# Performance work log

Measured on AMD Instinct MI355X. Metric: run time of the kernel, lower is better.

## Reference

```python
import jax, jax.numpy as jnp
import numpy as np

N_NODES = 50000
IN_DIM = 256
OUT_DIM = 128
NNZ_FEAT = 800000
NNZ_ADJ = 800000


def setup_inputs() -> dict:
    key = jax.random.key(0)
    ks = jax.random.split(key, 10)
    inp = {
        "feat_row": jax.random.randint(ks[0], (NNZ_FEAT,), 0, N_NODES, dtype=jnp.int32),
        "feat_col": jax.random.randint(ks[1], (NNZ_FEAT,), 0, IN_DIM, dtype=jnp.int32),
        "feat_vals": jnp.ones((NNZ_FEAT,), dtype=jnp.float32),  # binary features (int-cast in original)
        "adj1_row": jax.random.randint(ks[2], (NNZ_ADJ,), 0, N_NODES, dtype=jnp.int32),
        "adj1_col": jax.random.randint(ks[3], (NNZ_ADJ,), 0, N_NODES, dtype=jnp.int32),
        "adj1_vals": jax.random.uniform(ks[4], (NNZ_ADJ,), dtype=jnp.float32),
        "adj2_row": jax.random.randint(ks[5], (NNZ_ADJ,), 0, N_NODES, dtype=jnp.int32),
        "adj2_col": jax.random.randint(ks[6], (NNZ_ADJ,), 0, N_NODES, dtype=jnp.int32),
        "adj2_vals": jax.random.uniform(ks[7], (NNZ_ADJ,), dtype=jnp.float32),
    }
    # Glorot-uniform weights as in weight_variable_glorot
    lim = np.sqrt(6.0 / (IN_DIM + OUT_DIM))
    inp["W1"] = jax.random.uniform(ks[8], (IN_DIM, OUT_DIM), minval=-lim, maxval=lim, dtype=jnp.float32)
    inp["W2"] = jax.random.uniform(ks[9], (IN_DIM, OUT_DIM), minval=-lim, maxval=lim, dtype=jnp.float32)
    inp["n_nodes"] = N_NODES
    return inp


def _spmm_feat(row, col, vals, W, n_nodes):
    # X (sparse [N, F]) @ W ([F, D]) -> [N, D]
    msg = vals[:, None] * W[col]  # [nnz, D]
    return jax.ops.segment_sum(msg, row, num_segments=n_nodes)


def _spmm_adj(row, col, vals, H, n_nodes):
    # A (sparse [N, N]) @ H ([N, D]) -> [N, D]
    msg = vals[:, None] * H[col]  # [E, D]
    return jax.ops.segment_sum(msg, row, num_segments=n_nodes)


def reference(feat_row, feat_col, feat_vals, adj1_row, adj1_col, adj1_vals,
              adj2_row, adj2_col, adj2_vals, W1, W2, n_nodes):
    # dropout=0.0 -> keep_prob=1 -> sparse dropout is identity with scale 1.0
    xw1 = _spmm_feat(feat_row, feat_col, feat_vals, W1, n_nodes)   # [N, D]
    x1 = _spmm_adj(adj1_row, adj1_col, adj1_vals, xw1, n_nodes)    # [N, D]
    xw2 = _spmm_feat(feat_row, feat_col, feat_vals, W2, n_nodes)
    x2 = _spmm_adj(adj2_row, adj2_col, adj2_vals, xw2, n_nodes)
    return jax.nn.relu(x1 + x2)
```

## Files before the change

### kernel.cpp

```cpp
#include <hip/hip_runtime.h>
#include <hip/hip_fp16.h>

#define N_NODES 50000
#define IN_DIM 256
#define OUT_DIM 128
#define NNZ 800000
#define SCAN_N (3 * N_NODES)
#define TOTAL_NNZ (3 * NNZ)
#define SCAN_BLOCKS ((SCAN_N + 255) / 256)
#define NPART 8
#define PART_W (N_NODES / NPART)

#define BCAP 310016

#define NSUB 64
#define SUBW 98
#define SUBCAP 6144
#define ENT_B 4096
#define BBLK_B ((BCAP + ENT_B - 1) / ENT_B)

#define ADJ_SL 4
#define ADJ_RC ((N_NODES + 63) / 64)

typedef float vf4 __attribute__((ext_vector_type(4)));

static __device__ __forceinline__ unsigned pack_cv(int c, float v) {
    return ((unsigned)c << 16) | (unsigned)__half_as_ushort(__float2half(v));
}
static __device__ __forceinline__ int   upk_c(unsigned pk) { return (int)(pk >> 16); }
static __device__ __forceinline__ float upk_v(unsigned pk) {
    return __half2float(__ushort_as_half((unsigned short)(pk & 0xffffu)));
}
static __device__ __forceinline__ float h2f(unsigned short h) {
    return __half2float(__ushort_as_half(h));
}

__global__ void bucket_kernel(const int* __restrict__ fr, const int* __restrict__ fc,
                              const float* __restrict__ fv,
                              const int* __restrict__ a1r, const int* __restrict__ a1c,
                              const float* __restrict__ a1v,
                              const int* __restrict__ a2r, const int* __restrict__ a2c,
                              const float* __restrict__ a2v,
                              int* __restrict__ bcur,
                              unsigned* __restrict__ gpack,
                              unsigned short* __restrict__ gmeta) {
    __shared__ int cnt8[8];
    __shared__ int offc[8];
    __shared__ int gbase[8];
    __shared__ unsigned spk[768];
    __shared__ unsigned short smeta[768];
    int t = threadIdx.x;
    if (t < 8) cnt8[t] = 0;
    __syncthreads();

    int e = blockIdx.x * 256 + t;
    int r[3]; unsigned pk[3]; int loc[3]; int pb[3];
    r[0] = __builtin_nontemporal_load(&fr[e]);
    pk[0] = pack_cv(__builtin_nontemporal_load(&fc[e]),
                    __builtin_nontemporal_load(&fv[e]));
    r[1] = __builtin_nontemporal_load(&a1r[e]);
    pk[1] = pack_cv(__builtin_nontemporal_load(&a1c[e]),
                    __builtin_nontemporal_load(&a1v[e]));
    r[2] = __builtin_nontemporal_load(&a2r[e]);
    pk[2] = pack_cv(__builtin_nontemporal_load(&a2c[e]),
                    __builtin_nontemporal_load(&a2v[e]));
#pragma unroll
    for (int s = 0; s < 3; ++s) {
        pb[s] = r[s] / PART_W;
        loc[s] = atomicAdd(&cnt8[pb[s]], 1);
    }
    __syncthreads();
    if (t < 8) gbase[t] = atomicAdd(&bcur[t], cnt8[t]);
    if (t == 0) {
        int acc = 0;
#pragma unroll
        for (int q = 0; q < 8; ++q) { offc[q] = acc; acc += cnt8[q]; }
    }
    __syncthreads();
#pragma unroll
    for (int s = 0; s < 3; ++s) {
        int pos = offc[pb[s]] + loc[s];
        spk[pos] = pk[s];
        smeta[pos] = (unsigned short)((s << 13) | (r[s] - pb[s] * PART_W));
    }
    __syncthreads();
#pragma unroll
    for (int k = 0; k < 3; ++k) {
        int i = t + k * 256;
        int q = 0;
#pragma unroll
        for (int b = 1; b < 8; ++b) q += (i >= offc[b]);
        int g = q * BCAP + gbase[q] + (i - offc[q]);
        gpack[g] = spk[i];
        gmeta[g] = smeta[i];
    }
}

__global__ void subbucket_kernel(const unsigned* __restrict__ gpack1,
                                 const unsigned short* __restrict__ gmeta1,
                                 const int* __restrict__ bcur,
                                 int* __restrict__ subcur,
                                 unsigned* __restrict__ gpack2,
                                 unsigned short* __restrict__ gmeta2) {
    int p = blockIdx.x & (NPART - 1);
    int chunk = blockIdx.x >> 3;
    int base = chunk * ENT_B;
    int n = bcur[p];
    int cnt = n - base;
    if (cnt <= 0) return;
    if (cnt > ENT_B) cnt = ENT_B;
    __shared__ int c64[NSUB], off[NSUB], gb[NSUB];
    __shared__ unsigned spk[ENT_B];
    __shared__ unsigned short smt[ENT_B];
    int t = threadIdx.x;
    if (t < NSUB) c64[t] = 0;
    __syncthreads();
    unsigned pk[16]; unsigned short mt[16]; int loc[16]; int sb[16];
#pragma unroll
    for (int k = 0; k < 16; ++k) {
        int i = t + k * 256;
        if (i < cnt) {
            pk[k] = gpack1[p * BCAP + base + i];
            mt[k] = gmeta1[p * BCAP + base + i];
            sb[k] = (int)(mt[k] & 8191u) / SUBW;
            loc[k] = atomicAdd(&c64[sb[k]], 1);
        } else sb[k] = -1;
    }
    __syncthreads();
    if (t == 0) {
        int a = 0;
#pragma unroll
        for (int q = 0; q < NSUB; ++q) { off[q] = a; a += c64[q]; }
    }
    __syncthreads();
    if (t < NSUB && c64[t] > 0) gb[t] = atomicAdd(&subcur[p * NSUB + t], c64[t]);
    __syncthreads();
#pragma unroll
    for (int k = 0; k < 16; ++k) {
        if (sb[k] >= 0) {
            int pos = off[sb[k]] + loc[k];
            spk[pos] = pk[k];
            smt[pos] = mt[k];
        }
    }
    __syncthreads();
    for (int i = t; i < cnt; i += 256) {
        unsigned short m = smt[i];
        int s2 = (int)(m & 8191u) / SUBW;
        int g = (p * NSUB + s2) * SUBCAP + gb[s2] + (i - off[s2]);
        gpack2[g] = spk[i];
        gmeta2[g] = m;
    }
}

__global__ __launch_bounds__(512) void subhist_kernel(
        const unsigned short* __restrict__ gmeta2,
        const int* __restrict__ subcur,
        int* __restrict__ cnt) {
    int p = blockIdx.x & (NPART - 1);
    int sub = blockIdx.x >> 3;
    int n = subcur[p * NSUB + sub];
    __shared__ int h[512];
    int t = threadIdx.x;
    h[t] = 0;
    __syncthreads();
    long base = (long)(p * NSUB + sub) * SUBCAP;
    for (int i = t; i < n; i += 512) {
        unsigned short m = gmeta2[base + i];
        int key = (int)(m >> 13) * SUBW + ((int)(m & 8191u) - sub * SUBW);
        atomicAdd(&h[key], 1);
    }
    __syncthreads();
    if (t < 3 * SUBW) {
        int s = t / SUBW, d = t - s * SUBW;
        int rl = sub * SUBW + d;
        if (rl < PART_W) cnt[s * N_NODES + p * PART_W + rl] = h[t];
    }
}

__global__ void scan_block_kernel(const int* __restrict__ cnt,
                                  int* __restrict__ starts,
                                  int* __restrict__ bsum) {
    __shared__ int tmp[256];
    int g = blockIdx.x * 256 + threadIdx.x;
    int v = (g < SCAN_N) ? cnt[g] : 0;
    tmp[threadIdx.x] = v;
    __syncthreads();
    for (int off = 1; off < 256; off <<= 1) {
        int t = (threadIdx.x >= off) ? tmp[threadIdx.x - off] : 0;
        __syncthreads();
        tmp[threadIdx.x] += t;
        __syncthreads();
    }
    int incl = tmp[threadIdx.x];
    if (g < SCAN_N) starts[g] = incl - v;
    if (threadIdx.x == 255) bsum[blockIdx.x] = incl;
}

__global__ void scan_bsum_kernel(int* __restrict__ bsum, int nb) {
    __shared__ int tmp[1024];
    int t = threadIdx.x;
    int v = (t < nb) ? bsum[t] : 0;
    tmp[t] = v;
    __syncthreads();
    for (int off = 1; off < 1024; off <<= 1) {
        int x = (t >= off) ? tmp[t - off] : 0;
        __syncthreads();
        tmp[t] += x;
        __syncthreads();
    }
    if (t < nb) bsum[t] = tmp[t] - v;
}

__global__ void scan_add_kernel(int* __restrict__ starts,
                                const int* __restrict__ bsum) {
    int g = blockIdx.x * 256 + threadIdx.x;
    if (g < SCAN_N) starts[g] += bsum[blockIdx.x];
}

__global__ __launch_bounds__(512) void sort_write_kernel(
        const unsigned* __restrict__ gpack2,
        const unsigned short* __restrict__ gmeta2,
        const int* __restrict__ subcur,
        const int* __restrict__ starts,
        unsigned* __restrict__ spack) {
    int p = blockIdx.x & (NPART - 1);
    int sub = blockIdx.x >> 3;
    int n = subcur[p * NSUB + sub];
    __shared__ int h[512];
    __shared__ int e[512];
    __shared__ int cur[512];
    __shared__ unsigned sorted[SUBCAP];
    int t = threadIdx.x;
    h[t] = 0;
    __syncthreads();
    long base = (long)(p * NSUB + sub) * SUBCAP;
    unsigned pk[12]; short ky[12];
#pragma unroll
    for (int k = 0; k < 12; ++k) {
        int i = t + k * 512;
        if (i < n) {
            pk[k] = gpack2[base + i];
            unsigned short m = gmeta2[base + i];
            int key = (int)(m >> 13) * SUBW + ((int)(m & 8191u) - sub * SUBW);
            ky[k] = (short)key;
            atomicAdd(&h[key], 1);
        } else ky[k] = -1;
    }
    __syncthreads();
    e[t] = h[t];
    __syncthreads();
    for (int off = 1; off < 512; off <<= 1) {
        int v = (t >= off) ? e[t - off] : 0;
        __syncthreads();
        e[t] += v;
        __syncthreads();
    }
    int excl = e[t] - h[t];
    __syncthreads();
    e[t] = excl;
    cur[t] = excl;
    __syncthreads();
#pragma unroll
    for (int k = 0; k < 12; ++k) {
        if (ky[k] >= 0) {
            int pos = atomicAdd(&cur[ky[k]], 1);
            sorted[pos] = pk[k];
        }
    }
    __syncthreads();
    int s1 = e[SUBW];
    int s2 = e[2 * SUBW];
    int rb = p * PART_W + sub * SUBW;
    int gb0 = starts[rb];
    int gb1 = starts[N_NODES + rb];
    int gb2 = starts[2 * N_NODES + rb];
#pragma unroll
    for (int k = 0; k < 12; ++k) {
        int i = t + k * 512;
        if (i < n) {
            unsigned v = sorted[i];
            int dst;
            if (i < s1)      dst = gb0 + i;
            else if (i < s2) dst = gb1 + (i - s1);
            else             dst = gb2 + (i - s2);
            spack[dst] = v;
        }
    }
}

__global__ void feat_gather_kernel(const int* __restrict__ starts,
                                   const unsigned* __restrict__ spack,
                                   const float4* __restrict__ W1,
                                   const float4* __restrict__ W2,
                                   ushort4* __restrict__ xw1s,
                                   ushort4* __restrict__ xw2s) {
    int lane = threadIdx.x & 31;
    int sub  = threadIdx.x >> 5;
    int r = blockIdx.x * 8 + sub;
    if (r >= N_NODES) return;
    int s = starts[r];
    int e = starts[r + 1];
    float4 a1 = make_float4(0.f, 0.f, 0.f, 0.f);
    float4 a2 = make_float4(0.f, 0.f, 0.f, 0.f);
    for (int base = s; base < e; base += 32) {
        int n = e - base;
        int m = (n < 32) ? n : 32;
        unsigned pk = (lane < m) ? spack[base + lane] : 0u;
        int j = 0;
        for (; j + 7 < m; j += 8) {
            unsigned pp[8]; float4 w1v[8]; float4 w2v[8];
#pragma unroll
            for (int k = 0; k < 8; ++k) pp[k] = __shfl(pk, j + k, 32);
#pragma unroll
            for (int k = 0; k < 8; ++k) {
                int c = upk_c(pp[k]);
                w1v[k] = W1[c * 32 + lane];
                w2v[k] = W2[c * 32 + lane];
            }
#pragma unroll
            for (int k = 0; k < 8; ++k) {
                float v = upk_v(pp[k]);
                a1.x += v * w1v[k].x; a1.y += v * w1v[k].y;
                a1.z += v * w1v[k].z; a1.w += v * w1v[k].w;
                a2.x += v * w2v[k].x; a2.y += v * w2v[k].y;
                a2.z += v * w2v[k].z; a2.w += v * w2v[k].w;
            }
        }
        for (; j + 3 < m; j += 4) {
            unsigned pp[4]; float4 w1v[4]; float4 w2v[4];
#pragma unroll
            for (int k = 0; k < 4; ++k) pp[k] = __shfl(pk, j + k, 32);
#pragma unroll
            for (int k = 0; k < 4; ++k) {
                int c = upk_c(pp[k]);
                w1v[k] = W1[c * 32 + lane];
                w2v[k] = W2[c * 32 + lane];
            }
#pragma unroll
            for (int k = 0; k < 4; ++k) {
                float v = upk_v(pp[k]);
                a1.x += v * w1v[k].x; a1.y += v * w1v[k].y;
                a1.z += v * w1v[k].z; a1.w += v * w1v[k].w;
                a2.x += v * w2v[k].x; a2.y += v * w2v[k].y;
                a2.z += v * w2v[k].z; a2.w += v * w2v[k].w;
            }
        }
        for (; j < m; ++j) {
            unsigned pj = __shfl(pk, j, 32);
            int c = upk_c(pj);
            float v = upk_v(pj);
            float4 w1 = W1[c * 32 + lane];
            float4 w2 = W2[c * 32 + lane];
            a1.x += v * w1.x; a1.y += v * w1.y; a1.z += v * w1.z; a1.w += v * w1.w;
            a2.x += v * w2.x; a2.y += v * w2.y; a2.z += v * w2.z; a2.w += v * w2.w;
        }
    }
    ushort4 q1, q2;
    q1.x = __half_as_ushort(__float2half(a1.x)); q1.y = __half_as_ushort(__float2half(a1.y));
    q1.z = __half_as_ushort(__float2half(a1.z)); q1.w = __half_as_ushort(__float2half(a1.w));
    q2.x = __half_as_ushort(__float2half(a2.x)); q2.y = __half_as_ushort(__float2half(a2.y));
    q2.z = __half_as_ushort(__float2half(a2.z)); q2.w = __half_as_ushort(__float2half(a2.w));
    size_t idx = (size_t)(lane >> 3) * (N_NODES * 8) + (size_t)r * 8 + (lane & 7);
    xw1s[idx] = q1;
    xw2s[idx] = q2;
}

__global__ __launch_bounds__(512) void adj_pass_rel0(
        const int* __restrict__ starts,
        const unsigned* __restrict__ spack,
        const ushort4* __restrict__ xws,
        vf4* __restrict__ out) {
    int s  = blockIdx.x & (ADJ_SL - 1);
    int rc = blockIdx.x >> 2;
    int g  = threadIdx.x >> 3;
    int q  = threadIdx.x & 7;
    int r  = rc * 64 + g;
    bool valid = (r < N_NODES);
    vf4 acc = {0.f, 0.f, 0.f, 0.f};
    const ushort4* __restrict__ sl = xws + (size_t)s * (N_NODES * 8);
    size_t oidx = (size_t)r * 32 + s * 8 + q;

    int st = 0, en = 0;
    if (valid) {
        st = starts[N_NODES + r];
        en = starts[N_NODES + r + 1];
    }
    for (int base = st; base < en; base += 16) {
        int m = en - base;
        unsigned pk0 = (q < m)     ? spack[base + q]     : 0u;
        unsigned pk1 = (8 + q < m) ? spack[base + 8 + q] : 0u;
        {
            unsigned pp[8]; ushort4 xx[8];
#pragma unroll
            for (int k = 0; k < 8; ++k) pp[k] = __shfl(pk0, k, 8);
#pragma unroll
            for (int k = 0; k < 8; ++k) xx[k] = sl[upk_c(pp[k]) * 8 + q];
#pragma unroll
            for (int k = 0; k < 8; ++k) {
                float v = upk_v(pp[k]);
                acc.x += v * h2f(xx[k].x); acc.y += v * h2f(xx[k].y);
                acc.z += v * h2f(xx[k].z); acc.w += v * h2f(xx[k].w);
            }
        }
        if (m <= 8) continue;
        {
            unsigned pp[8]; ushort4 xx[8];
#pragma unroll
            for (int k = 0; k < 8; ++k) pp[k] = __shfl(pk1, k, 8);
#pragma unroll
            for (int k = 0; k < 8; ++k) xx[k] = sl[upk_c(pp[k]) * 8 + q];
#pragma unroll
            for (int k = 0; k < 8; ++k) {
                float v = upk_v(pp[k]);
                acc.x += v * h2f(xx[k].x); acc.y += v * h2f(xx[k].y);
                acc.z += v * h2f(xx[k].z); acc.w += v * h2f(xx[k].w);
            }
        }
    }
    if (valid) __builtin_nontemporal_store(acc, &out[oidx]);
}

__global__ __launch_bounds__(512) void adj_pass_rel1(
        const int* __restrict__ starts,
        const unsigned* __restrict__ spack,
        const ushort4* __restrict__ xws,
        vf4* __restrict__ out) {
    int s  = blockIdx.x & (ADJ_SL - 1);
    int rc = blockIdx.x >> 2;
    int g  = threadIdx.x >> 3;
    int q  = threadIdx.x & 7;
    int r  = rc * 64 + g;
    bool valid = (r < N_NODES);
    vf4 acc = {0.f, 0.f, 0.f, 0.f};
    const ushort4* __restrict__ sl = xws + (size_t)s * (N_NODES * 8);
    size_t oidx = (size_t)r * 32 + s * 8 + q;

    int st = 0, en = 0;
    if (valid) {
        st = starts[2 * N_NODES + r];
        en = (r == N_NODES - 1) ? TOTAL_NNZ : starts[2 * N_NODES + r + 1];
    }
    vf4 prev = {0.f, 0.f, 0.f, 0.f};
    if (valid) prev = __builtin_nontemporal_load(&out[oidx]);

    for (int base = st; base < en; base += 16) {
        int m = en - base;
        unsigned pk0 = (q < m)     ? spack[base + q]     : 0u;
        unsigned pk1 = (8 + q < m) ? spack[base + 8 + q] : 0u;
        {
            unsigned pp[8]; ushort4 xx[8];
#pragma unroll
            for (int k = 0; k < 8; ++k) pp[k] = __shfl(pk0, k, 8);
#pragma unroll
            for (int k = 0; k < 8; ++k) xx[k] = sl[upk_c(pp[k]) * 8 + q];
#pragma unroll
            for (int k = 0; k < 8; ++k) {
                float v = upk_v(pp[k]);
                acc.x += v * h2f(xx[k].x); acc.y += v * h2f(xx[k].y);
                acc.z += v * h2f(xx[k].z); acc.w += v * h2f(xx[k].w);
            }
        }
        if (m <= 8) continue;
        {
            unsigned pp[8]; ushort4 xx[8];
#pragma unroll
            for (int k = 0; k < 8; ++k) pp[k] = __shfl(pk1, k, 8);
#pragma unroll
            for (int k = 0; k < 8; ++k) xx[k] = sl[upk_c(pp[k]) * 8 + q];
#pragma unroll
            for (int k = 0; k < 8; ++k) {
                float v = upk_v(pp[k]);
                acc.x += v * h2f(xx[k].x); acc.y += v * h2f(xx[k].y);
                acc.z += v * h2f(xx[k].z); acc.w += v * h2f(xx[k].w);
            }
        }
    }
    if (valid) {
        vf4 res;
        res.x = fmaxf(acc.x + prev.x, 0.f);
        res.y = fmaxf(acc.y + prev.y, 0.f);
        res.z = fmaxf(acc.z + prev.z, 0.f);
        res.w = fmaxf(acc.w + prev.w, 0.f);
        __builtin_nontemporal_store(res, &out[oidx]);
    }
}

extern "C" void kernel_launch(void* const* d_in, const int* in_sizes, int n_in,
                              void* d_out, int out_size, void* d_ws, size_t ws_size,
                              hipStream_t stream) {
    const int*   feat_row  = (const int*)  d_in[0];
    const int*   feat_col  = (const int*)  d_in[1];
    const float* feat_vals = (const float*)d_in[2];
    const int*   adj1_row  = (const int*)  d_in[3];
    const int*   adj1_col  = (const int*)  d_in[4];
    const float* adj1_vals = (const float*)d_in[5];
    const int*   adj2_row  = (const int*)  d_in[6];
    const int*   adj2_col  = (const int*)  d_in[7];
    const float* adj2_vals = (const float*)d_in[8];
    const float* W1        = (const float*)d_in[9];
    const float* W2        = (const float*)d_in[10];

    char* ws = (char*)d_ws;
    unsigned* spack = (unsigned*)ws;            ws += (size_t)TOTAL_NNZ * 4;
    int*      cnt   = (int*)ws;                 ws += (size_t)SCAN_N * 4;
    int*      starts= (int*)ws;                 ws += (size_t)SCAN_N * 4;
    int*      bsum  = (int*)ws;                 ws += 1024 * 4;
    int*      bcur  = (int*)ws;                 ws += 16 * 4;
    int*      subcur= (int*)ws;                 ws += (size_t)NPART * NSUB * 4;
    char*     bkt   = ws;
    unsigned* gpack1 = (unsigned*)bkt;
    unsigned short* gmeta1 = (unsigned short*)(bkt + (size_t)NPART * BCAP * 4);
    unsigned* gpack2 = (unsigned*)(bkt + (size_t)NPART * BCAP * 6);
    unsigned short* gmeta2 = (unsigned short*)(bkt + (size_t)NPART * BCAP * 6
                                                  + (size_t)NPART * NSUB * SUBCAP * 4);
    ushort4*  xw1s  = (ushort4*)bkt;
    ushort4*  xw2s  = (ushort4*)(bkt + (size_t)N_NODES * OUT_DIM * 2);

    (void)hipMemsetAsync(bcur, 0, (16 + NPART * NSUB) * sizeof(int), stream);

    const int block = 256;

    bucket_kernel<<<NNZ / block, block, 0, stream>>>(
        feat_row, feat_col, feat_vals,
        adj1_row, adj1_col, adj1_vals,
        adj2_row, adj2_col, adj2_vals,
        bcur, gpack1, gmeta1);

    subbucket_kernel<<<NPART * BBLK_B, block, 0, stream>>>(
        gpack1, gmeta1, bcur, subcur, gpack2, gmeta2);

    subhist_kernel<<<NPART * NSUB, 512, 0, stream>>>(gmeta2, subcur, cnt);

    scan_block_kernel<<<SCAN_BLOCKS, 256, 0, stream>>>(cnt, starts, bsum);
    scan_bsum_kernel<<<1, 1024, 0, stream>>>(bsum, SCAN_BLOCKS);
    scan_add_kernel<<<SCAN_BLOCKS, 256, 0, stream>>>(starts, bsum);

    sort_write_kernel<<<NPART * NSUB, 512, 0, stream>>>(
        gpack2, gmeta2, subcur, starts, spack);

    const int grid_rows = N_NODES / 8;
    feat_gather_kernel<<<grid_rows, 256, 0, stream>>>(
        starts, spack, (const float4*)W1, (const float4*)W2, xw1s, xw2s);

    adj_pass_rel0<<<ADJ_SL * ADJ_RC, 512, 0, stream>>>(
        starts, spack, xw1s, (vf4*)d_out);
    adj_pass_rel1<<<ADJ_SL * ADJ_RC, 512, 0, stream>>>(
        starts, spack, xw2s, (vf4*)d_out);
}
```

Measured before the change: 264.9 us.

## Densify feature matrix and compute X@W with MFMA instead of sparse gather

The sparse feature matrix is scattered with atomics into a dense fp32 N×256 buffer, and X@[W1|W2] is computed with fp16 MFMA 16x16x32 instructions. Feature nonzeros no longer go through the bucket/sort pipeline, which now handles only the two adjacency relations, so the buckets and scan are smaller. In exchange it adds a 51 MB memset, an atomic scatter and a dense GEMM read of that buffer. It also rounds X to fp16, which is exact for the binary test features but lossy for general values.

```diff
diff --git a/kernel.cpp b/kernel.cpp
--- a/kernel.cpp
+++ b/kernel.cpp
@@ -5,17 +5,17 @@
 #define IN_DIM 256
 #define OUT_DIM 128
 #define NNZ 800000
-#define SCAN_N (3 * N_NODES)
-#define TOTAL_NNZ (3 * NNZ)
+#define N_ADJ_TOT (2 * NNZ)
+#define SCAN_N (2 * N_NODES)
 #define SCAN_BLOCKS ((SCAN_N + 255) / 256)
 #define NPART 8
 #define PART_W (N_NODES / NPART)
 
-#define BCAP 310016
+#define BCAP 208128
 
 #define NSUB 64
 #define SUBW 98
-#define SUBCAP 6144
+#define SUBCAP 4096
 #define ENT_B 4096
 #define BBLK_B ((BCAP + ENT_B - 1) / ENT_B)
 
@@ -23,6 +23,8 @@
 #define ADJ_RC ((N_NODES + 63) / 64)
 
 typedef float vf4 __attribute__((ext_vector_type(4)));
+typedef float f32x4a __attribute__((ext_vector_type(4)));
+typedef _Float16 f16x8 __attribute__((ext_vector_type(8)));
 
 static __device__ __forceinline__ unsigned pack_cv(int c, float v) {
     return ((unsigned)c << 16) | (unsigned)__half_as_ushort(__float2half(v));
@@ -35,9 +37,83 @@
     return __half2float(__ushort_as_half(h));
 }
 
-__global__ void bucket_kernel(const int* __restrict__ fr, const int* __restrict__ fc,
-                              const float* __restrict__ fv,
-                              const int* __restrict__ a1r, const int* __restrict__ a1c,
+__global__ void densify_kernel(const int* __restrict__ fr,
+                               const int* __restrict__ fc,
+                               const float* __restrict__ fv,
+                               float* __restrict__ X) {
+    int e = blockIdx.x * 256 + threadIdx.x;
+    int r = __builtin_nontemporal_load(&fr[e]);
+    int c = __builtin_nontemporal_load(&fc[e]);
+    float v = __builtin_nontemporal_load(&fv[e]);
+    atomicAdd(&X[(size_t)r * IN_DIM + c], v);
+}
+
+__global__ void bprep_kernel(const float* __restrict__ W1,
+                             const float* __restrict__ W2,
+                             f16x8* __restrict__ Bfrag) {
+    int idx = blockIdx.x * 256 + threadIdx.x;
+    int tk = idx >> 6, l = idx & 63;
+    int ct = tk >> 3, kk = tk & 7;
+    int col = ct * 16 + (l & 15);
+    int kb = kk * 32 + ((l >> 4) << 3);
+    f16x8 b;
+#pragma unroll
+    for (int i = 0; i < 8; ++i) {
+        int k = kb + i;
+        float w = (col < OUT_DIM) ? W1[k * OUT_DIM + col]
+                                  : W2[k * OUT_DIM + (col - OUT_DIM)];
+        b[i] = (_Float16)w;
+    }
+    Bfrag[tk * 64 + l] = b;
+}
+
+__global__ __launch_bounds__(256) void feat_mfma_kernel(
+        const float* __restrict__ X,
+        const f16x8* __restrict__ Bfrag,
+        __half* __restrict__ xw1h,
+        __half* __restrict__ xw2h) {
+    int r0 = blockIdx.x * 16;
+    int w = threadIdx.x >> 6, l = threadIdx.x & 63;
+    f32x4a acc0 = {0.f,0.f,0.f,0.f}, acc1 = {0.f,0.f,0.f,0.f};
+    f32x4a acc2 = {0.f,0.f,0.f,0.f}, acc3 = {0.f,0.f,0.f,0.f};
+    int row = r0 + (l & 15);
+    const float* ap = X + (size_t)row * IN_DIM + ((l >> 4) << 3);
+#pragma unroll
+    for (int kk = 0; kk < 8; ++kk) {
+        const float4* a4 = (const float4*)(ap + kk * 32);
+        float4 x0 = a4[0];
+        float4 x1 = a4[1];
+        f16x8 a;
+        a[0] = (_Float16)x0.x; a[1] = (_Float16)x0.y;
+        a[2] = (_Float16)x0.z; a[3] = (_Float16)x0.w;
+        a[4] = (_Float16)x1.x; a[5] = (_Float16)x1.y;
+        a[6] = (_Float16)x1.z; a[7] = (_Float16)x1.w;
+        f16x8 b0 = Bfrag[((4 * w + 0) * 8 + kk) * 64 + l];
+        f16x8 b1 = Bfrag[((4 * w + 1) * 8 + kk) * 64 + l];
+        f16x8 b2 = Bfrag[((4 * w + 2) * 8 + kk) * 64 + l];
+        f16x8 b3 = Bfrag[((4 * w + 3) * 8 + kk) * 64 + l];
+        acc0 = __builtin_amdgcn_mfma_f32_16x16x32_f16(a, b0, acc0, 0, 0, 0);
+        acc1 = __builtin_amdgcn_mfma_f32_16x16x32_f16(a, b1, acc1, 0, 0, 0);
+        acc2 = __builtin_amdgcn_mfma_f32_16x16x32_f16(a, b2, acc2, 0, 0, 0);
+        acc3 = __builtin_amdgcn_mfma_f32_16x16x32_f16(a, b3, acc3, 0, 0, 0);
+    }
+#pragma unroll
+    for (int ct = 0; ct < 4; ++ct) {
+        f32x4a acc = (ct == 0) ? acc0 : (ct == 1) ? acc1 : (ct == 2) ? acc2 : acc3;
+        int col = (4 * w + ct) * 16 + (l & 15);
+        int dim = col & (OUT_DIM - 1);
+        __half* base = (col < OUT_DIM) ? xw1h : xw2h;
+        int slice = dim >> 5, within = dim & 31;
+        size_t sb = (size_t)slice * N_NODES * 32 + within;
+#pragma unroll
+        for (int j = 0; j < 4; ++j) {
+            int rr = r0 + ((l >> 4) << 2) + j;
+            base[sb + (size_t)rr * 32] = __float2half(acc[j]);
+        }
+    }
+}
+
+__global__ void bucket_kernel(const int* __restrict__ a1r, const int* __restrict__ a1c,
                               const float* __restrict__ a1v,
                               const int* __restrict__ a2r, const int* __restrict__ a2c,
                               const float* __restrict__ a2v,
@@ -47,25 +123,22 @@
     __shared__ int cnt8[8];
     __shared__ int offc[8];
     __shared__ int gbase[8];
-    __shared__ unsigned spk[768];
-    __shared__ unsigned short smeta[768];
+    __shared__ unsigned spk[512];
+    __shared__ unsigned short smeta[512];
     int t = threadIdx.x;
     if (t < 8) cnt8[t] = 0;
     __syncthreads();
 
     int e = blockIdx.x * 256 + t;
-    int r[3]; unsigned pk[3]; int loc[3]; int pb[3];
-    r[0] = __builtin_nontemporal_load(&fr[e]);
-    pk[0] = pack_cv(__builtin_nontemporal_load(&fc[e]),
-                    __builtin_nontemporal_load(&fv[e]));
-    r[1] = __builtin_nontemporal_load(&a1r[e]);
-    pk[1] = pack_cv(__builtin_nontemporal_load(&a1c[e]),
+    int r[2]; unsigned pk[2]; int loc[2]; int pb[2];
+    r[0] = __builtin_nontemporal_load(&a1r[e]);
+    pk[0] = pack_cv(__builtin_nontemporal_load(&a1c[e]),
                     __builtin_nontemporal_load(&a1v[e]));
-    r[2] = __builtin_nontemporal_load(&a2r[e]);
-    pk[2] = pack_cv(__builtin_nontemporal_load(&a2c[e]),
+    r[1] = __builtin_nontemporal_load(&a2r[e]);
+    pk[1] = pack_cv(__builtin_nontemporal_load(&a2c[e]),
                     __builtin_nontemporal_load(&a2v[e]));
 #pragma unroll
-    for (int s = 0; s < 3; ++s) {
+    for (int s = 0; s < 2; ++s) {
         pb[s] = r[s] / PART_W;
         loc[s] = atomicAdd(&cnt8[pb[s]], 1);
     }
@@ -78,14 +151,14 @@
     }
     __syncthreads();
 #pragma unroll
-    for (int s = 0; s < 3; ++s) {
+    for (int s = 0; s < 2; ++s) {
         int pos = offc[pb[s]] + loc[s];
         spk[pos] = pk[s];
         smeta[pos] = (unsigned short)((s << 13) | (r[s] - pb[s] * PART_W));
     }
     __syncthreads();
 #pragma unroll
-    for (int k = 0; k < 3; ++k) {
+    for (int k = 0; k < 2; ++k) {
         int i = t + k * 256;
         int q = 0;
 #pragma unroll
@@ -171,7 +244,7 @@
         atomicAdd(&h[key], 1);
     }
     __syncthreads();
-    if (t < 3 * SUBW) {
+    if (t < 2 * SUBW) {
         int s = t / SUBW, d = t - s * SUBW;
         int rl = sub * SUBW + d;
         if (rl < PART_W) cnt[s * N_NODES + p * PART_W + rl] = h[t];
@@ -235,9 +308,9 @@
     h[t] = 0;
     __syncthreads();
     long base = (long)(p * NSUB + sub) * SUBCAP;
-    unsigned pk[12]; short ky[12];
-#pragma unroll
-    for (int k = 0; k < 12; ++k) {
+    unsigned pk[8]; short ky[8];
+#pragma unroll
+    for (int k = 0; k < 8; ++k) {
         int i = t + k * 512;
         if (i < n) {
             pk[k] = gpack2[base + i];
@@ -262,7 +335,7 @@
     cur[t] = excl;
     __syncthreads();
 #pragma unroll
-    for (int k = 0; k < 12; ++k) {
+    for (int k = 0; k < 8; ++k) {
         if (ky[k] >= 0) {
             int pos = atomicAdd(&cur[ky[k]], 1);
             sorted[pos] = pk[k];
@@ -270,100 +343,18 @@
     }
     __syncthreads();
     int s1 = e[SUBW];
-    int s2 = e[2 * SUBW];
     int rb = p * PART_W + sub * SUBW;
     int gb0 = starts[rb];
     int gb1 = starts[N_NODES + rb];
-    int gb2 = starts[2 * N_NODES + rb];
-#pragma unroll
-    for (int k = 0; k < 12; ++k) {
+#pragma unroll
+    for (int k = 0; k < 8; ++k) {
         int i = t + k * 512;
         if (i < n) {
             unsigned v = sorted[i];
-            int dst;
-            if (i < s1)      dst = gb0 + i;
-            else if (i < s2) dst = gb1 + (i - s1);
-            else             dst = gb2 + (i - s2);
+            int dst = (i < s1) ? (gb0 + i) : (gb1 + (i - s1));
             spack[dst] = v;
         }
     }
-}
-
-__global__ void feat_gather_kernel(const int* __restrict__ starts,
-                                   const unsigned* __restrict__ spack,
-                                   const float4* __restrict__ W1,
-                                   const float4* __restrict__ W2,
-                                   ushort4* __restrict__ xw1s,
-                                   ushort4* __restrict__ xw2s) {
-    int lane = threadIdx.x & 31;
-    int sub  = threadIdx.x >> 5;
-    int r = blockIdx.x * 8 + sub;
-    if (r >= N_NODES) return;
-    int s = starts[r];
-    int e = starts[r + 1];
-    float4 a1 = make_float4(0.f, 0.f, 0.f, 0.f);
-    float4 a2 = make_float4(0.f, 0.f, 0.f, 0.f);
-    for (int base = s; base < e; base += 32) {
-        int n = e - base;
-        int m = (n < 32) ? n : 32;
-        unsigned pk = (lane < m) ? spack[base + lane] : 0u;
-        int j = 0;
-        for (; j + 7 < m; j += 8) {
-            unsigned pp[8]; float4 w1v[8]; float4 w2v[8];
-#pragma unroll
-            for (int k = 0; k < 8; ++k) pp[k] = __shfl(pk, j + k, 32);
-#pragma unroll
-            for (int k = 0; k < 8; ++k) {
-                int c = upk_c(pp[k]);
-                w1v[k] = W1[c * 32 + lane];
-                w2v[k] = W2[c * 32 + lane];
-            }
-#pragma unroll
-            for (int k = 0; k < 8; ++k) {
-                float v = upk_v(pp[k]);
-                a1.x += v * w1v[k].x; a1.y += v * w1v[k].y;
-                a1.z += v * w1v[k].z; a1.w += v * w1v[k].w;
-                a2.x += v * w2v[k].x; a2.y += v * w2v[k].y;
-                a2.z += v * w2v[k].z; a2.w += v * w2v[k].w;
-            }
-        }
-        for (; j + 3 < m; j += 4) {
-            unsigned pp[4]; float4 w1v[4]; float4 w2v[4];
-#pragma unroll
-            for (int k = 0; k < 4; ++k) pp[k] = __shfl(pk, j + k, 32);
-#pragma unroll
-            for (int k = 0; k < 4; ++k) {
-                int c = upk_c(pp[k]);
-                w1v[k] = W1[c * 32 + lane];
-                w2v[k] = W2[c * 32 + lane];
-            }
-#pragma unroll
-            for (int k = 0; k < 4; ++k) {
-                float v = upk_v(pp[k]);
-                a1.x += v * w1v[k].x; a1.y += v * w1v[k].y;
-                a1.z += v * w1v[k].z; a1.w += v * w1v[k].w;
-                a2.x += v * w2v[k].x; a2.y += v * w2v[k].y;
-                a2.z += v * w2v[k].z; a2.w += v * w2v[k].w;
-            }
-        }
-        for (; j < m; ++j) {
-            unsigned pj = __shfl(pk, j, 32);
-            int c = upk_c(pj);
-            float v = upk_v(pj);
-            float4 w1 = W1[c * 32 + lane];
-            float4 w2 = W2[c * 32 + lane];
-            a1.x += v * w1.x; a1.y += v * w1.y; a1.z += v * w1.z; a1.w += v * w1.w;
-            a2.x += v * w2.x; a2.y += v * w2.y; a2.z += v * w2.z; a2.w += v * w2.w;
-        }
-    }
-    ushort4 q1, q2;
-    q1.x = __half_as_ushort(__float2half(a1.x)); q1.y = __half_as_ushort(__float2half(a1.y));
-    q1.z = __half_as_ushort(__float2half(a1.z)); q1.w = __half_as_ushort(__float2half(a1.w));
-    q2.x = __half_as_ushort(__float2half(a2.x)); q2.y = __half_as_ushort(__float2half(a2.y));
-    q2.z = __half_as_ushort(__float2half(a2.z)); q2.w = __half_as_ushort(__float2half(a2.w));
-    size_t idx = (size_t)(lane >> 3) * (N_NODES * 8) + (size_t)r * 8 + (lane & 7);
-    xw1s[idx] = q1;
-    xw2s[idx] = q2;
 }
 
 __global__ __launch_bounds__(512) void adj_pass_rel0(
@@ -383,8 +374,8 @@
 
     int st = 0, en = 0;
     if (valid) {
-        st = starts[N_NODES + r];
-        en = starts[N_NODES + r + 1];
+        st = starts[r];
+        en = starts[r + 1];
     }
     for (int base = st; base < en; base += 16) {
         int m = en - base;
@@ -438,8 +429,8 @@
 
     int st = 0, en = 0;
     if (valid) {
-        st = starts[2 * N_NODES + r];
-        en = (r == N_NODES - 1) ? TOTAL_NNZ : starts[2 * N_NODES + r + 1];
+        st = starts[N_NODES + r];
+        en = (r == N_NODES - 1) ? N_ADJ_TOT : starts[N_NODES + r + 1];
     }
     vf4 prev = {0.f, 0.f, 0.f, 0.f};
     if (valid) prev = __builtin_nontemporal_load(&out[oidx]);
@@ -502,49 +493,48 @@
     const float* W2        = (const float*)d_in[10];
 
     char* ws = (char*)d_ws;
-    unsigned* spack = (unsigned*)ws;            ws += (size_t)TOTAL_NNZ * 4;
+    unsigned* spack = (unsigned*)ws;            ws += (size_t)N_ADJ_TOT * 4;
     int*      cnt   = (int*)ws;                 ws += (size_t)SCAN_N * 4;
     int*      starts= (int*)ws;                 ws += (size_t)SCAN_N * 4;
     int*      bsum  = (int*)ws;                 ws += 1024 * 4;
     int*      bcur  = (int*)ws;                 ws += 16 * 4;
     int*      subcur= (int*)ws;                 ws += (size_t)NPART * NSUB * 4;
+    float*    X     = (float*)ws;               ws += (size_t)N_NODES * IN_DIM * 4;
+    f16x8*    Bfrag = (f16x8*)ws;               ws += (size_t)128 * 64 * 16;
     char*     bkt   = ws;
     unsigned* gpack1 = (unsigned*)bkt;
     unsigned short* gmeta1 = (unsigned short*)(bkt + (size_t)NPART * BCAP * 4);
     unsigned* gpack2 = (unsigned*)(bkt + (size_t)NPART * BCAP * 6);
     unsigned short* gmeta2 = (unsigned short*)(bkt + (size_t)NPART * BCAP * 6
                                                   + (size_t)NPART * NSUB * SUBCAP * 4);
-    ushort4*  xw1s  = (ushort4*)bkt;
-    ushort4*  xw2s  = (ushort4*)(bkt + (size_t)N_NODES * OUT_DIM * 2);
+    __half*   xw1h  = (__half*)bkt;
+    __half*   xw2h  = (__half*)(bkt + (size_t)N_NODES * OUT_DIM * 2);
 
     (void)hipMemsetAsync(bcur, 0, (16 + NPART * NSUB) * sizeof(int), stream);
+    (void)hipMemsetAsync(X, 0, (size_t)N_NODES * IN_DIM * sizeof(float), stream);
 
     const int block = 256;
 
+    densify_kernel<<<NNZ / block, block, 0, stream>>>(feat_row, feat_col, feat_vals, X);
+    bprep_kernel<<<32, block, 0, stream>>>(W1, W2, Bfrag);
+
     bucket_kernel<<<NNZ / block, block, 0, stream>>>(
-        feat_row, feat_col, feat_vals,
         adj1_row, adj1_col, adj1_vals,
         adj2_row, adj2_col, adj2_vals,
         bcur, gpack1, gmeta1);
-
     subbucket_kernel<<<NPART * BBLK_B, block, 0, stream>>>(
         gpack1, gmeta1, bcur, subcur, gpack2, gmeta2);
-
     subhist_kernel<<<NPART * NSUB, 512, 0, stream>>>(gmeta2, subcur, cnt);
-
     scan_block_kernel<<<SCAN_BLOCKS, 256, 0, stream>>>(cnt, starts, bsum);
     scan_bsum_kernel<<<1, 1024, 0, stream>>>(bsum, SCAN_BLOCKS);
     scan_add_kernel<<<SCAN_BLOCKS, 256, 0, stream>>>(starts, bsum);
-
     sort_write_kernel<<<NPART * NSUB, 512, 0, stream>>>(
         gpack2, gmeta2, subcur, starts, spack);
 
-    const int grid_rows = N_NODES / 8;
-    feat_gather_kernel<<<grid_rows, 256, 0, stream>>>(
-        starts, spack, (const float4*)W1, (const float4*)W2, xw1s, xw2s);
+    feat_mfma_kernel<<<N_NODES / 16, 256, 0, stream>>>(X, Bfrag, xw1h, xw2h);
 
     adj_pass_rel0<<<ADJ_SL * ADJ_RC, 512, 0, stream>>>(
-        starts, spack, xw1s, (vf4*)d_out);
+        starts, spack, (const ushort4*)xw1h, (vf4*)d_out);
     adj_pass_rel1<<<ADJ_SL * ADJ_RC, 512, 0, stream>>>(
-        starts, spack, xw2s, (vf4*)d_out);
-}
+        starts, spack, (const ushort4*)xw2h, (vf4*)d_out);
+}
```

Measured after the change: 314.6 us. 1.19x slower.

## Replace histogram and global prefix scan with atomic segment allocation in sort

Applied to the files above, without the earlier changes.

Removes the subhist kernel and the three-kernel global prefix scan. Each sort_write block now reserves space for its three relation segments through an atomicAdd on a global cursor, then writes per-row start offsets and row lengths itself. The consumer kernels read rowlen instead of starts[r+1]. This drops four launches and one pass over the metadata, but the order of blocks within each relation's output becomes nondeterministic, which only changes memory locality and not the results.

```diff
diff --git a/kernel.cpp b/kernel.cpp
--- a/kernel.cpp
+++ b/kernel.cpp
@@ -7,7 +7,6 @@
 #define NNZ 800000
 #define SCAN_N (3 * N_NODES)
 #define TOTAL_NNZ (3 * NNZ)
-#define SCAN_BLOCKS ((SCAN_N + 255) / 256)
 #define NPART 8
 #define PART_W (N_NODES / NPART)
 
@@ -153,76 +152,13 @@
     }
 }
 
-__global__ __launch_bounds__(512) void subhist_kernel(
-        const unsigned short* __restrict__ gmeta2,
-        const int* __restrict__ subcur,
-        int* __restrict__ cnt) {
-    int p = blockIdx.x & (NPART - 1);
-    int sub = blockIdx.x >> 3;
-    int n = subcur[p * NSUB + sub];
-    __shared__ int h[512];
-    int t = threadIdx.x;
-    h[t] = 0;
-    __syncthreads();
-    long base = (long)(p * NSUB + sub) * SUBCAP;
-    for (int i = t; i < n; i += 512) {
-        unsigned short m = gmeta2[base + i];
-        int key = (int)(m >> 13) * SUBW + ((int)(m & 8191u) - sub * SUBW);
-        atomicAdd(&h[key], 1);
-    }
-    __syncthreads();
-    if (t < 3 * SUBW) {
-        int s = t / SUBW, d = t - s * SUBW;
-        int rl = sub * SUBW + d;
-        if (rl < PART_W) cnt[s * N_NODES + p * PART_W + rl] = h[t];
-    }
-}
-
-__global__ void scan_block_kernel(const int* __restrict__ cnt,
-                                  int* __restrict__ starts,
-                                  int* __restrict__ bsum) {
-    __shared__ int tmp[256];
-    int g = blockIdx.x * 256 + threadIdx.x;
-    int v = (g < SCAN_N) ? cnt[g] : 0;
-    tmp[threadIdx.x] = v;
-    __syncthreads();
-    for (int off = 1; off < 256; off <<= 1) {
-        int t = (threadIdx.x >= off) ? tmp[threadIdx.x - off] : 0;
-        __syncthreads();
-        tmp[threadIdx.x] += t;
-        __syncthreads();
-    }
-    int incl = tmp[threadIdx.x];
-    if (g < SCAN_N) starts[g] = incl - v;
-    if (threadIdx.x == 255) bsum[blockIdx.x] = incl;
-}
-
-__global__ void scan_bsum_kernel(int* __restrict__ bsum, int nb) {
-    __shared__ int tmp[1024];
-    int t = threadIdx.x;
-    int v = (t < nb) ? bsum[t] : 0;
-    tmp[t] = v;
-    __syncthreads();
-    for (int off = 1; off < 1024; off <<= 1) {
-        int x = (t >= off) ? tmp[t - off] : 0;
-        __syncthreads();
-        tmp[t] += x;
-        __syncthreads();
-    }
-    if (t < nb) bsum[t] = tmp[t] - v;
-}
-
-__global__ void scan_add_kernel(int* __restrict__ starts,
-                                const int* __restrict__ bsum) {
-    int g = blockIdx.x * 256 + threadIdx.x;
-    if (g < SCAN_N) starts[g] += bsum[blockIdx.x];
-}
-
 __global__ __launch_bounds__(512) void sort_write_kernel(
         const unsigned* __restrict__ gpack2,
         const unsigned short* __restrict__ gmeta2,
         const int* __restrict__ subcur,
-        const int* __restrict__ starts,
+        int* __restrict__ cur3,
+        int* __restrict__ starts,
+        int* __restrict__ rowlen,
         unsigned* __restrict__ spack) {
     int p = blockIdx.x & (NPART - 1);
     int sub = blockIdx.x >> 3;
@@ -230,6 +166,8 @@
     __shared__ int h[512];
     __shared__ int e[512];
     __shared__ int cur[512];
+    __shared__ int segbase[4];
+    __shared__ int gbs[3];
     __shared__ unsigned sorted[SUBCAP];
     int t = threadIdx.x;
     h[t] = 0;
@@ -260,7 +198,17 @@
     __syncthreads();
     e[t] = excl;
     cur[t] = excl;
-    __syncthreads();
+    if (t == 0) {
+        segbase[0] = 0;
+    }
+    __syncthreads();
+    if (t == 0) {
+        segbase[1] = e[SUBW];
+        segbase[2] = e[2 * SUBW];
+        segbase[3] = n;
+    }
+    __syncthreads();
+    if (t < 3) gbs[t] = atomicAdd(&cur3[t], segbase[t + 1] - segbase[t]);
 #pragma unroll
     for (int k = 0; k < 12; ++k) {
         if (ky[k] >= 0) {
@@ -269,27 +217,28 @@
         }
     }
     __syncthreads();
-    int s1 = e[SUBW];
-    int s2 = e[2 * SUBW];
-    int rb = p * PART_W + sub * SUBW;
-    int gb0 = starts[rb];
-    int gb1 = starts[N_NODES + rb];
-    int gb2 = starts[2 * N_NODES + rb];
+    if (t < 3 * SUBW) {
+        int s = t / SUBW, d = t - s * SUBW;
+        int rl = sub * SUBW + d;
+        if (rl < PART_W) {
+            int gr = s * N_NODES + p * PART_W + rl;
+            starts[gr] = s * NNZ + gbs[s] + (e[t] - segbase[s]);
+            rowlen[gr] = h[t];
+        }
+    }
+    int s1 = segbase[1], s2 = segbase[2];
 #pragma unroll
     for (int k = 0; k < 12; ++k) {
         int i = t + k * 512;
         if (i < n) {
-            unsigned v = sorted[i];
-            int dst;
-            if (i < s1)      dst = gb0 + i;
-            else if (i < s2) dst = gb1 + (i - s1);
-            else             dst = gb2 + (i - s2);
-            spack[dst] = v;
+            int sg = (i < s1) ? 0 : ((i < s2) ? 1 : 2);
+            spack[sg * NNZ + gbs[sg] + (i - segbase[sg])] = sorted[i];
         }
     }
 }
 
 __global__ void feat_gather_kernel(const int* __restrict__ starts,
+                                   const int* __restrict__ rowlen,
                                    const unsigned* __restrict__ spack,
                                    const float4* __restrict__ W1,
                                    const float4* __restrict__ W2,
@@ -300,7 +249,7 @@
     int r = blockIdx.x * 8 + sub;
     if (r >= N_NODES) return;
     int s = starts[r];
-    int e = starts[r + 1];
+    int e = s + rowlen[r];
     float4 a1 = make_float4(0.f, 0.f, 0.f, 0.f);
     float4 a2 = make_float4(0.f, 0.f, 0.f, 0.f);
     for (int base = s; base < e; base += 32) {
@@ -368,6 +317,7 @@
 
 __global__ __launch_bounds__(512) void adj_pass_rel0(
         const int* __restrict__ starts,
+        const int* __restrict__ rowlen,
         const unsigned* __restrict__ spack,
         const ushort4* __restrict__ xws,
         vf4* __restrict__ out) {
@@ -384,7 +334,7 @@
     int st = 0, en = 0;
     if (valid) {
         st = starts[N_NODES + r];
-        en = starts[N_NODES + r + 1];
+        en = st + rowlen[N_NODES + r];
     }
     for (int base = st; base < en; base += 16) {
         int m = en - base;
@@ -423,6 +373,7 @@
 
 __global__ __launch_bounds__(512) void adj_pass_rel1(
         const int* __restrict__ starts,
+        const int* __restrict__ rowlen,
         const unsigned* __restrict__ spack,
         const ushort4* __restrict__ xws,
         vf4* __restrict__ out) {
@@ -439,7 +390,7 @@
     int st = 0, en = 0;
     if (valid) {
         st = starts[2 * N_NODES + r];
-        en = (r == N_NODES - 1) ? TOTAL_NNZ : starts[2 * N_NODES + r + 1];
+        en = st + rowlen[2 * N_NODES + r];
     }
     vf4 prev = {0.f, 0.f, 0.f, 0.f};
     if (valid) prev = __builtin_nontemporal_load(&out[oidx]);
@@ -503,11 +454,11 @@
 
     char* ws = (char*)d_ws;
     unsigned* spack = (unsigned*)ws;            ws += (size_t)TOTAL_NNZ * 4;
-    int*      cnt   = (int*)ws;                 ws += (size_t)SCAN_N * 4;
     int*      starts= (int*)ws;                 ws += (size_t)SCAN_N * 4;
-    int*      bsum  = (int*)ws;                 ws += 1024 * 4;
+    int*      rowlen= (int*)ws;                 ws += (size_t)SCAN_N * 4;
     int*      bcur  = (int*)ws;                 ws += 16 * 4;
     int*      subcur= (int*)ws;                 ws += (size_t)NPART * NSUB * 4;
+    int*      cur3  = (int*)ws;                 ws += 16 * 4;
     char*     bkt   = ws;
     unsigned* gpack1 = (unsigned*)bkt;
     unsigned short* gmeta1 = (unsigned short*)(bkt + (size_t)NPART * BCAP * 4);
@@ -517,7 +468,7 @@
     ushort4*  xw1s  = (ushort4*)bkt;
     ushort4*  xw2s  = (ushort4*)(bkt + (size_t)N_NODES * OUT_DIM * 2);
 
-    (void)hipMemsetAsync(bcur, 0, (16 + NPART * NSUB) * sizeof(int), stream);
+    (void)hipMemsetAsync(bcur, 0, (16 + NPART * NSUB + 16) * sizeof(int), stream);
 
     const int block = 256;
 
@@ -530,21 +481,15 @@
     subbucket_kernel<<<NPART * BBLK_B, block, 0, stream>>>(
         gpack1, gmeta1, bcur, subcur, gpack2, gmeta2);
 
-    subhist_kernel<<<NPART * NSUB, 512, 0, stream>>>(gmeta2, subcur, cnt);
-
-    scan_block_kernel<<<SCAN_BLOCKS, 256, 0, stream>>>(cnt, starts, bsum);
-    scan_bsum_kernel<<<1, 1024, 0, stream>>>(bsum, SCAN_BLOCKS);
-    scan_add_kernel<<<SCAN_BLOCKS, 256, 0, stream>>>(starts, bsum);
-
     sort_write_kernel<<<NPART * NSUB, 512, 0, stream>>>(
-        gpack2, gmeta2, subcur, starts, spack);
+        gpack2, gmeta2, subcur, cur3, starts, rowlen, spack);
 
     const int grid_rows = N_NODES / 8;
     feat_gather_kernel<<<grid_rows, 256, 0, stream>>>(
-        starts, spack, (const float4*)W1, (const float4*)W2, xw1s, xw2s);
+        starts, rowlen, spack, (const float4*)W1, (const float4*)W2, xw1s, xw2s);
 
     adj_pass_rel0<<<ADJ_SL * ADJ_RC, 512, 0, stream>>>(
-        starts, spack, xw1s, (vf4*)d_out);
+        starts, rowlen, spack, xw1s, (vf4*)d_out);
     adj_pass_rel1<<<ADJ_SL * ADJ_RC, 512, 0, stream>>>(
-        starts, spack, xw2s, (vf4*)d_out);
-}
+        starts, rowlen, spack, xw2s, (vf4*)d_out);
+}
```

New measurement: 259.5 us. 1.02x faster.
